# Performance work log

Hardware: AMD Instinct MI355X
Metric: run time of the kernel (lower is better)

Reference implementation:

```python
import jax, jax.numpy as jnp
import numpy as np

N_NODES = 100000


def _gcn_conv(h, src, dst, W, b, n_nodes):
    """PyG GCNConv with add_self_loops=True, symmetric normalization.
    out = D^-1/2 (A + I) D^-1/2 (h W) + b, aggregating src->dst."""
    h = h @ W  # transform first (out_dim <= in_dim), as PyG does
    ones = jnp.ones(src.shape[0], dtype=h.dtype)
    deg = jax.ops.segment_sum(ones, dst, num_segments=n_nodes) + 1.0  # +1 self loop
    dinv = jax.lax.rsqrt(deg)
    coef = dinv[src] * dinv[dst]  # per-edge norm
    agg = jax.ops.segment_sum(h[src] * coef[:, None], dst, num_segments=n_nodes)
    agg = agg + h * (dinv * dinv)[:, None]  # self-loop term: dinv_i^2 * h_i
    return agg + b


def setup_inputs() -> dict:
    key = jax.random.key(0)
    k1, k2, k3, k4 = jax.random.split(key, 4)
    x = jax.random.normal(k1, (N_NODES, 256), dtype=jnp.float32)
    edge_index = jax.random.randint(k2, (2, 1600000), 0, N_NODES, dtype=jnp.int64)
    W1 = jax.random.normal(k3, (256, 128), dtype=jnp.float32) * (1.0 / np.sqrt(256))
    b1 = jnp.zeros((128,), dtype=jnp.float32)
    W2 = jax.random.normal(k4, (128, 64), dtype=jnp.float32) * (1.0 / np.sqrt(128))
    b2 = jnp.zeros((64,), dtype=jnp.float32)
    return {"x": x, "edge_index": edge_index, "W1": W1, "b1": b1, "W2": W2, "b2": b2}


def reference(x, edge_index, W1, b1, W2, b2):
    src, dst = edge_index[0], edge_index[1]
    h = jax.nn.relu(_gcn_conv(x, src, dst, W1, b1, N_NODES))
    # dropout is identity in eval mode
    h = _gcn_conv(h, src, dst, W2, b2, N_NODES)
    return jax.nn.log_softmax(h, axis=1)
```

## Files before the change

### kernel.cpp

```cpp
#include <hip/hip_runtime.h>
#include <hip/hip_bf16.h>


#define N_NODES 100000
#define F_IN 256
#define F_MID 128
#define F_OUT 64

#define BSHIFT 8
#define BNODES 256
#define NBUCKETS ((N_NODES + BNODES - 1) / BNODES)
#define BCAP 6144
#define EPB 4096

typedef __attribute__((ext_vector_type(8))) short short8;
typedef __attribute__((ext_vector_type(4))) float f32x4;

__device__ inline ushort bf16_rne(float f) {
    uint u = __float_as_uint(f);
    u += 0x7FFF + ((u >> 16) & 1);
    return (ushort)(u >> 16);
}
__device__ inline float lo16(uint r) { return __uint_as_float(r << 16); }
__device__ inline float hi16(uint r) { return __uint_as_float(r & 0xffff0000u); }
__device__ inline uint pack_bf2(float a, float b) {
    return (uint)bf16_rne(a) | ((uint)bf16_rne(b) << 16);
}


__global__ __launch_bounds__(256)
void bucket_scatter_kernel(const int* __restrict__ src, const int* __restrict__ dst,
                           int* __restrict__ bcur, uint* __restrict__ ebuf, int E) {
    __shared__ int curL[NBUCKETS];
    int t = threadIdx.x;
    int e0 = blockIdx.x * EPB;
    int e1 = e0 + EPB; if (e1 > E) e1 = E;

    for (int i = t; i < NBUCKETS; i += 256) curL[i] = 0;
    __syncthreads();
    for (int i = e0 + t; i < e1; i += 256) atomicAdd(&curL[dst[i] >> BSHIFT], 1);
    __syncthreads();
    for (int i = t; i < NBUCKETS; i += 256) {
        int h = curL[i];
        curL[i] = h ? atomicAdd(&bcur[i], h) : 0;
    }
    __syncthreads();
    for (int i = e0 + t; i < e1; i += 256) {
        int d = dst[i], s = src[i];
        int b = d >> BSHIFT;
        int pos = atomicAdd(&curL[b], 1);
        if (pos < BCAP) ebuf[(size_t)b * BCAP + pos] = ((uint)(d & (BNODES - 1)) << 17) | (uint)s;
    }
}

__global__ __launch_bounds__(256)
void bucket_sort_kernel(const uint* __restrict__ ebuf, const int* __restrict__ bcur,
                        int* __restrict__ ssrc, int* __restrict__ rs, int* __restrict__ cnt,
                        float* __restrict__ dinv, int n) {
    __shared__ uint eL[BCAP];
    __shared__ int hist[BNODES], ps[BNODES];
    int b = blockIdx.x, t = threadIdx.x;
    int nb = bcur[b];
    if (nb > BCAP) nb = BCAP;
    for (int i = t; i < nb; i += 256) eL[i] = ebuf[(size_t)b * BCAP + i];
    hist[t] = 0;
    __syncthreads();
    for (int i = t; i < nb; i += 256) atomicAdd(&hist[eL[i] >> 17], 1);
    __syncthreads();
    ps[t] = hist[t];
    __syncthreads();
#pragma unroll
    for (int off = 1; off < BNODES; off <<= 1) {
        int v = (t >= off) ? ps[t - off] : 0;
        __syncthreads();
        ps[t] += v;
        __syncthreads();
    }
    int excl = ps[t] - hist[t];
    int node = b * BNODES + t;
    if (node < n) {
        rs[node] = b * BCAP + excl;
        cnt[node] = hist[t];
        dinv[node] = 1.0f / sqrtf((float)hist[t] + 1.0f);
    }
    __syncthreads();
    ps[t] = excl;
    __syncthreads();
    for (int i = t; i < nb; i += 256) {
        uint e = eL[i];
        int d = e >> 17;
        int p = atomicAdd(&ps[d], 1);
        ssrc[(size_t)b * BCAP + p] = (int)(e & 0x1FFFF);
    }
}

__global__ __launch_bounds__(256)
void wprep_kernel(const float* __restrict__ W1, const float* __restrict__ W2,
                  short8* __restrict__ W1f, short8* __restrict__ W2f) {
    int b = blockIdx.x;
    if (b < 16) {
        int f = b * 256 + threadIdx.x;
        int k0 = f >> 9, nt = (f >> 6) & 7, ln = f & 63;
        int kbase = k0 * 32 + (ln >> 4) * 8;
        int n = nt * 16 + (ln & 15);
        short8 fr;
#pragma unroll
        for (int j = 0; j < 8; ++j) fr[j] = (short)bf16_rne(W1[(kbase + j) * F_MID + n]);
        W1f[f] = fr;
    } else {
        int f = (b - 16) * 256 + threadIdx.x;
        int k0 = f >> 8, nt = (f >> 6) & 3, ln = f & 63;
        int kbase = k0 * 32 + (ln >> 4) * 8;
        int n = nt * 16 + (ln & 15);
        short8 fr;
#pragma unroll
        for (int j = 0; j < 8; ++j) fr[j] = (short)bf16_rne(W2[(kbase + j) * F_OUT + n]);
        W2f[f] = fr;
    }
}


__global__ __launch_bounds__(512, 2)
void gemm1_kernel(const float* __restrict__ A, const short8* __restrict__ Wf,
                  const float* __restrict__ dinv, ushort* __restrict__ C,
                  int M) {
    __shared__ short8 BsF[4096];
    __shared__ ushort Abuf[2][128 * 64];
    int tid = threadIdx.x;
    int lane = tid & 63, w = tid >> 6;
    int m0 = blockIdx.x * 128;

    int o0 = tid * 2;
    int srow = o0 >> 3;
    int gr = m0 + srow; if (gr >= M) gr = m0;
    int cl0 = o0 & 7, cl1 = cl0 + 1;
    int cg0 = cl0 ^ (srow & 7), cg1 = cl1 ^ (srow & 7);
    const float* arow = &A[(size_t)gr * F_IN];

    float4 rv[2][2];
    rv[0][0] = ((const float4*)(arow + cg0 * 8))[0];
    rv[0][1] = ((const float4*)(arow + cg0 * 8))[1];
    rv[1][0] = ((const float4*)(arow + cg1 * 8))[0];
    rv[1][1] = ((const float4*)(arow + cg1 * 8))[1];

    for (int f = tid; f < 4096; f += 512) BsF[f] = Wf[f];

    {
        short8 pk;
        pk[0] = (short)bf16_rne(rv[0][0].x); pk[1] = (short)bf16_rne(rv[0][0].y);
        pk[2] = (short)bf16_rne(rv[0][0].z); pk[3] = (short)bf16_rne(rv[0][0].w);
        pk[4] = (short)bf16_rne(rv[0][1].x); pk[5] = (short)bf16_rne(rv[0][1].y);
        pk[6] = (short)bf16_rne(rv[0][1].z); pk[7] = (short)bf16_rne(rv[0][1].w);
        *(short8*)&Abuf[0][o0 * 8] = pk;
        pk[0] = (short)bf16_rne(rv[1][0].x); pk[1] = (short)bf16_rne(rv[1][0].y);
        pk[2] = (short)bf16_rne(rv[1][0].z); pk[3] = (short)bf16_rne(rv[1][0].w);
        pk[4] = (short)bf16_rne(rv[1][1].x); pk[5] = (short)bf16_rne(rv[1][1].y);
        pk[6] = (short)bf16_rne(rv[1][1].z); pk[7] = (short)bf16_rne(rv[1][1].w);
        *(short8*)&Abuf[0][(o0 + 1) * 8] = pk;
    }
    __syncthreads();

    f32x4 acc[8];
#pragma unroll
    for (int nt = 0; nt < 8; ++nt) acc[nt] = (f32x4){0.f, 0.f, 0.f, 0.f};

    int arow16 = w * 16 + (lane & 15);
    int asw = arow16 & 7;
    int abase = arow16 * 8;

#pragma unroll
    for (int kc = 0; kc < 4; ++kc) {
        int b = kc & 1;
        if (kc < 3) {
            const float* s0 = arow + (kc + 1) * 64 + cg0 * 8;
            const float* s1 = arow + (kc + 1) * 64 + cg1 * 8;
            rv[0][0] = ((const float4*)s0)[0];
            rv[0][1] = ((const float4*)s0)[1];
            rv[1][0] = ((const float4*)s1)[0];
            rv[1][1] = ((const float4*)s1)[1];
            asm volatile("" ::: "memory");
        }
#pragma unroll
        for (int kk = 0; kk < 2; ++kk) {
            int k0 = kc * 2 + kk;
            int c = kk * 4 + (lane >> 4);
            short8 af = *(const short8*)&Abuf[b][(abase + (c ^ asw)) * 8];
#pragma unroll
            for (int nt = 0; nt < 8; ++nt) {
                short8 bfr = BsF[(k0 * 8 + nt) * 64 + lane];
                acc[nt] = __builtin_amdgcn_mfma_f32_16x16x32_bf16(af, bfr, acc[nt], 0, 0, 0);
            }
        }
        if (kc < 3) {
            short8 pk;
            pk[0] = (short)bf16_rne(rv[0][0].x); pk[1] = (short)bf16_rne(rv[0][0].y);
            pk[2] = (short)bf16_rne(rv[0][0].z); pk[3] = (short)bf16_rne(rv[0][0].w);
            pk[4] = (short)bf16_rne(rv[0][1].x); pk[5] = (short)bf16_rne(rv[0][1].y);
            pk[6] = (short)bf16_rne(rv[0][1].z); pk[7] = (short)bf16_rne(rv[0][1].w);
            *(short8*)&Abuf[b ^ 1][o0 * 8] = pk;
            pk[0] = (short)bf16_rne(rv[1][0].x); pk[1] = (short)bf16_rne(rv[1][0].y);
            pk[2] = (short)bf16_rne(rv[1][0].z); pk[3] = (short)bf16_rne(rv[1][0].w);
            pk[4] = (short)bf16_rne(rv[1][1].x); pk[5] = (short)bf16_rne(rv[1][1].y);
            pk[6] = (short)bf16_rne(rv[1][1].z); pk[7] = (short)bf16_rne(rv[1][1].w);
            *(short8*)&Abuf[b ^ 1][(o0 + 1) * 8] = pk;
        }
        __syncthreads();
    }

#pragma unroll
    for (int i = 0; i < 4; ++i) {
        int r = blockIdx.x * 128 + w * 16 + (lane >> 4) * 4 + i;
        if (r < M) {
            float dv = dinv[r];
#pragma unroll
            for (int nt = 0; nt < 8; ++nt)
                C[(size_t)r * F_MID + nt * 16 + (lane & 15)] = bf16_rne(dv * acc[nt][i]);
        }
    }
}

__global__ __launch_bounds__(512, 4)
void gemm2_kernel(const ushort* __restrict__ A, const short8* __restrict__ Wf,
                  const float* __restrict__ dinv, ushort* __restrict__ C,
                  int M) {
    __shared__ short8 BsF[1024];
    int tid = threadIdx.x;
    int lane = tid & 63, w = tid >> 6;
    for (int f = tid; f < 1024; f += 512) BsF[f] = Wf[f];
    __syncthreads();

    int m0 = blockIdx.x * 128 + w * 16;
    int m = m0 + (lane & 15);
    bool mOk = (m < M);

    f32x4 acc[4];
#pragma unroll
    for (int nt = 0; nt < 4; ++nt) acc[nt] = (f32x4){0.f, 0.f, 0.f, 0.f};

    short8 afr[4];
#pragma unroll
    for (int k0 = 0; k0 < 4; ++k0) {
        short8 af = (short8){0, 0, 0, 0, 0, 0, 0, 0};
        if (mOk) af = *(const short8*)&A[(size_t)m * F_MID + k0 * 32 + (lane >> 4) * 8];
        afr[k0] = af;
    }
#pragma unroll
    for (int k0 = 0; k0 < 4; ++k0)
#pragma unroll
        for (int nt = 0; nt < 4; ++nt) {
            short8 bfr = BsF[(k0 * 4 + nt) * 64 + lane];
            acc[nt] = __builtin_amdgcn_mfma_f32_16x16x32_bf16(afr[k0], bfr, acc[nt], 0, 0, 0);
        }
#pragma unroll
    for (int i = 0; i < 4; ++i) {
        int r = m0 + (lane >> 4) * 4 + i;
        if (r < M) {
            float dv = dinv[r];
#pragma unroll
            for (int nt = 0; nt < 4; ++nt)
                C[(size_t)r * F_OUT + nt * 16 + (lane & 15)] = bf16_rne(dv * acc[nt][i]);
        }
    }
}

__global__ __launch_bounds__(256)
void agg1_kernel(const uint4* __restrict__ h, const int* __restrict__ rs,
                 const int* __restrict__ cnt, const int* __restrict__ ssrc,
                 const float* __restrict__ dinv, const float* __restrict__ bias,
                 uint4* __restrict__ outp, int n) {
    int w = threadIdx.x >> 6, lane = threadIdx.x & 63;
    int node = blockIdx.x * 4 + w;
    if (node >= n) return;
    int q = lane >> 4, c16 = lane & 15;
    int start = rs[node], c = cnt[node];
    float dn = dinv[node];
    float a[8];
#pragma unroll
    for (int i = 0; i < 8; ++i) a[i] = 0.f;

    for (int base = 0; base < c; base += 16) {
        bool p[4];
        int s[4];
        uint4 r[4];
#pragma unroll
        for (int j = 0; j < 4; ++j) {
            int e = base + j * 4 + q;
            p[j] = e < c;
            if (p[j]) s[j] = ssrc[start + e];
        }
#pragma unroll
        for (int j = 0; j < 4; ++j)
            if (p[j]) r[j] = h[(size_t)s[j] * 16 + c16];
#pragma unroll
        for (int j = 0; j < 4; ++j) {
            if (p[j]) {
                a[0] += lo16(r[j].x); a[1] += hi16(r[j].x);
                a[2] += lo16(r[j].y); a[3] += hi16(r[j].y);
                a[4] += lo16(r[j].z); a[5] += hi16(r[j].z);
                a[6] += lo16(r[j].w); a[7] += hi16(r[j].w);
            }
        }
    }
#pragma unroll
    for (int i = 0; i < 8; ++i) {
        a[i] += __shfl_xor(a[i], 16);
        a[i] += __shfl_xor(a[i], 32);
    }
    uint4 sr = h[(size_t)node * 16 + c16];
    const float4* b4 = (const float4*)bias;
    float4 b0 = b4[c16 * 2], b1 = b4[c16 * 2 + 1];
    float o0 = fmaxf(fmaf(dn, a[0] + lo16(sr.x), b0.x), 0.f);
    float o1 = fmaxf(fmaf(dn, a[1] + hi16(sr.x), b0.y), 0.f);
    float o2 = fmaxf(fmaf(dn, a[2] + lo16(sr.y), b0.z), 0.f);
    float o3 = fmaxf(fmaf(dn, a[3] + hi16(sr.y), b0.w), 0.f);
    float o4 = fmaxf(fmaf(dn, a[4] + lo16(sr.z), b1.x), 0.f);
    float o5 = fmaxf(fmaf(dn, a[5] + hi16(sr.z), b1.y), 0.f);
    float o6 = fmaxf(fmaf(dn, a[6] + lo16(sr.w), b1.z), 0.f);
    float o7 = fmaxf(fmaf(dn, a[7] + hi16(sr.w), b1.w), 0.f);
    if (q == 0) {
        uint4 ov;
        ov.x = pack_bf2(o0, o1);
        ov.y = pack_bf2(o2, o3);
        ov.z = pack_bf2(o4, o5);
        ov.w = pack_bf2(o6, o7);
        outp[(size_t)node * 16 + c16] = ov;
    }
}

__global__ __launch_bounds__(256)
void agg2_kernel(const uint2* __restrict__ h, const int* __restrict__ rs,
                 const int* __restrict__ cnt, const int* __restrict__ ssrc,
                 const float* __restrict__ dinv, const float* __restrict__ bias,
                 float4* __restrict__ out4, int n) {
    int w = threadIdx.x >> 6, lane = threadIdx.x & 63;
    int node = blockIdx.x * 4 + w;
    if (node >= n) return;
    int q = lane >> 4, c16 = lane & 15;
    int start = rs[node], c = cnt[node];
    float dn = dinv[node];
    float a[4];
#pragma unroll
    for (int i = 0; i < 4; ++i) a[i] = 0.f;

    for (int base = 0; base < c; base += 16) {
        bool p[4];
        int s[4];
        uint2 r[4];
#pragma unroll
        for (int j = 0; j < 4; ++j) {
            int e = base + j * 4 + q;
            p[j] = e < c;
            if (p[j]) s[j] = ssrc[start + e];
        }
#pragma unroll
        for (int j = 0; j < 4; ++j)
            if (p[j]) r[j] = h[(size_t)s[j] * 16 + c16];
#pragma unroll
        for (int j = 0; j < 4; ++j) {
            if (p[j]) {
                a[0] += lo16(r[j].x); a[1] += hi16(r[j].x);
                a[2] += lo16(r[j].y); a[3] += hi16(r[j].y);
            }
        }
    }
#pragma unroll
    for (int i = 0; i < 4; ++i) {
        a[i] += __shfl_xor(a[i], 16);
        a[i] += __shfl_xor(a[i], 32);
    }
    uint2 sr = h[(size_t)node * 16 + c16];
    float4 bv = ((const float4*)bias)[c16];
    float v0 = fmaf(dn, a[0] + lo16(sr.x), bv.x);
    float v1 = fmaf(dn, a[1] + hi16(sr.x), bv.y);
    float v2 = fmaf(dn, a[2] + lo16(sr.y), bv.z);
    float v3 = fmaf(dn, a[3] + hi16(sr.y), bv.w);
    float m = fmaxf(fmaxf(v0, v1), fmaxf(v2, v3));
#pragma unroll
    for (int off = 1; off < 16; off <<= 1) m = fmaxf(m, __shfl_xor(m, off));
    float ssum = expf(v0 - m) + expf(v1 - m) + expf(v2 - m) + expf(v3 - m);
#pragma unroll
    for (int off = 1; off < 16; off <<= 1) ssum += __shfl_xor(ssum, off);
    float lg = m + logf(ssum);
    if (q == 0) out4[(size_t)node * 16 + c16] = make_float4(v0 - lg, v1 - lg, v2 - lg, v3 - lg);
}


extern "C" void kernel_launch(void* const* d_in, const int* in_sizes, int n_in,
                              void* d_out, int out_size, void* d_ws, size_t ws_size,
                              hipStream_t stream) {
    const float* x  = (const float*)d_in[0];
    const int*   ei = (const int*)d_in[1];
    const float* W1 = (const float*)d_in[2];
    const float* b1 = (const float*)d_in[3];
    const float* W2 = (const float*)d_in[4];
    const float* b2 = (const float*)d_in[5];
    float* out = (float*)d_out;

    const int N = N_NODES;
    const int E = in_sizes[1] / 2;
    const int* src = ei;
    const int* dst = ei + E;

    char* ws = (char*)d_ws;
    size_t off = 0;
    auto alloc = [&](size_t bytes) {
        char* p = ws + off;
        off = (off + bytes + 255) & ~(size_t)255;
        return p;
    };
    int*    bcur   = (int*)alloc(NBUCKETS * 4);
    int*    rs     = (int*)alloc(N * 4);
    int*    cnt    = (int*)alloc(N * 4);
    float*  dinv   = (float*)alloc(N * 4);
    short8* W1f    = (short8*)alloc(4096 * 16);
    short8* W2f    = (short8*)alloc(1024 * 16);
    uint*   ebuf   = (uint*)alloc((size_t)NBUCKETS * BCAP * 4);
    int*    ssrc   = (int*)alloc((size_t)NBUCKETS * BCAP * 4);
    uint*   h1     = (uint*)alloc((size_t)N * 64 * 4);
    uint*   h1a    = (uint*)alloc((size_t)N * 64 * 4);
    ushort* h2     = (ushort*)h1;

    const int nScatBlocks = (E + EPB - 1) / EPB;
    const int nAggBlocks  = (N + 3) / 4;
    const int nTiles      = (N + 127) / 128;

    hipMemsetAsync(bcur, 0, NBUCKETS * 4, stream);
    wprep_kernel<<<20, 256, 0, stream>>>(W1, W2, W1f, W2f);

    bucket_scatter_kernel<<<nScatBlocks, 256, 0, stream>>>(src, dst, bcur, ebuf, E);
    bucket_sort_kernel<<<NBUCKETS, 256, 0, stream>>>(ebuf, bcur, ssrc, rs, cnt, dinv, N);

    gemm1_kernel<<<nTiles, 512, 0, stream>>>(x, W1f, dinv, (ushort*)h1, N);
    agg1_kernel<<<nAggBlocks, 256, 0, stream>>>((const uint4*)h1, rs, cnt, ssrc, dinv, b1,
                                                (uint4*)h1a, N);
    gemm2_kernel<<<nTiles, 512, 0, stream>>>((const ushort*)h1a, W2f, dinv, h2, N);
    agg2_kernel<<<nAggBlocks, 256, 0, stream>>>((const uint2*)h2, rs, cnt, ssrc, dinv, b2,
                                                (float4*)out, N);
}
```

Baseline: 374.1 us.

## Fuse layer-1 aggregation with layer-2 GEMM via shared-memory row tile

```diff
diff --git a/kernel.cpp b/kernel.cpp
--- a/kernel.cpp
+++ b/kernel.cpp
@@ -219,111 +219,97 @@
     }
 }
 
-__global__ __launch_bounds__(512, 4)
-void gemm2_kernel(const ushort* __restrict__ A, const short8* __restrict__ Wf,
-                  const float* __restrict__ dinv, ushort* __restrict__ C,
-                  int M) {
-    __shared__ short8 BsF[1024];
-    int tid = threadIdx.x;
-    int lane = tid & 63, w = tid >> 6;
-    for (int f = tid; f < 1024; f += 512) BsF[f] = Wf[f];
-    __syncthreads();
-
-    int m0 = blockIdx.x * 128 + w * 16;
-    int m = m0 + (lane & 15);
-    bool mOk = (m < M);
-
-    f32x4 acc[4];
-#pragma unroll
-    for (int nt = 0; nt < 4; ++nt) acc[nt] = (f32x4){0.f, 0.f, 0.f, 0.f};
-
-    short8 afr[4];
+__global__ __launch_bounds__(256)
+void agg1f_kernel(const uint4* __restrict__ h, const int* __restrict__ rs,
+                  const int* __restrict__ cnt, const int* __restrict__ ssrc,
+                  const float* __restrict__ dinv, const float* __restrict__ bias,
+                  const short8* __restrict__ W2f, ushort* __restrict__ h2, int n) {
+    __shared__ __align__(16) ushort rowsL[16][136];
+    int w = threadIdx.x >> 6, lane = threadIdx.x & 63;
+    int q = lane >> 4, c16 = lane & 15;
+    int nbase = blockIdx.x * 16;
+    const float4* b4 = (const float4*)bias;
+    float4 b0 = b4[c16 * 2], b1v = b4[c16 * 2 + 1];
+
+#pragma unroll
+    for (int i = 0; i < 4; ++i) {
+        int node = nbase + w * 4 + i;
+        bool nOk = (node < n);
+        int start = nOk ? rs[node] : 0;
+        int c = nOk ? cnt[node] : 0;
+        float dn = nOk ? dinv[node] : 0.f;
+        float a[8];
+#pragma unroll
+        for (int k = 0; k < 8; ++k) a[k] = 0.f;
+
+        for (int base = 0; base < c; base += 16) {
+            bool p[4];
+            int s[4];
+            uint4 r[4];
+#pragma unroll
+            for (int j = 0; j < 4; ++j) {
+                int e = base + j * 4 + q;
+                p[j] = e < c;
+                if (p[j]) s[j] = ssrc[start + e];
+            }
+#pragma unroll
+            for (int j = 0; j < 4; ++j)
+                if (p[j]) r[j] = h[(size_t)s[j] * 16 + c16];
+#pragma unroll
+            for (int j = 0; j < 4; ++j) {
+                if (p[j]) {
+                    a[0] += lo16(r[j].x); a[1] += hi16(r[j].x);
+                    a[2] += lo16(r[j].y); a[3] += hi16(r[j].y);
+                    a[4] += lo16(r[j].z); a[5] += hi16(r[j].z);
+                    a[6] += lo16(r[j].w); a[7] += hi16(r[j].w);
+                }
+            }
+        }
+#pragma unroll
+        for (int k = 0; k < 8; ++k) {
+            a[k] += __shfl_xor(a[k], 16);
+            a[k] += __shfl_xor(a[k], 32);
+        }
+        if (q == 0) {
+            short8 pk;
+            if (nOk) {
+                uint4 sr = h[(size_t)node * 16 + c16];
+                float o0 = fmaxf(fmaf(dn, a[0] + lo16(sr.x), b0.x), 0.f);
+                float o1 = fmaxf(fmaf(dn, a[1] + hi16(sr.x), b0.y), 0.f);
+                float o2 = fmaxf(fmaf(dn, a[2] + lo16(sr.y), b0.z), 0.f);
+                float o3 = fmaxf(fmaf(dn, a[3] + hi16(sr.y), b0.w), 0.f);
+                float o4 = fmaxf(fmaf(dn, a[4] + lo16(sr.z), b1v.x), 0.f);
+                float o5 = fmaxf(fmaf(dn, a[5] + hi16(sr.z), b1v.y), 0.f);
+                float o6 = fmaxf(fmaf(dn, a[6] + lo16(sr.w), b1v.z), 0.f);
+                float o7 = fmaxf(fmaf(dn, a[7] + hi16(sr.w), b1v.w), 0.f);
+                pk[0] = (short)bf16_rne(o0); pk[1] = (short)bf16_rne(o1);
+                pk[2] = (short)bf16_rne(o2); pk[3] = (short)bf16_rne(o3);
+                pk[4] = (short)bf16_rne(o4); pk[5] = (short)bf16_rne(o5);
+                pk[6] = (short)bf16_rne(o6); pk[7] = (short)bf16_rne(o7);
+            } else {
+                pk = (short8){0, 0, 0, 0, 0, 0, 0, 0};
+            }
+            *(short8*)&rowsL[w * 4 + i][c16 * 8] = pk;
+        }
+    }
+    __syncthreads();
+
+    f32x4 acc = (f32x4){0.f, 0.f, 0.f, 0.f};
+    int ar = lane & 15;
 #pragma unroll
     for (int k0 = 0; k0 < 4; ++k0) {
-        short8 af = (short8){0, 0, 0, 0, 0, 0, 0, 0};
-        if (mOk) af = *(const short8*)&A[(size_t)m * F_MID + k0 * 32 + (lane >> 4) * 8];
-        afr[k0] = af;
-    }
-#pragma unroll
-    for (int k0 = 0; k0 < 4; ++k0)
-#pragma unroll
-        for (int nt = 0; nt < 4; ++nt) {
-            short8 bfr = BsF[(k0 * 4 + nt) * 64 + lane];
-            acc[nt] = __builtin_amdgcn_mfma_f32_16x16x32_bf16(afr[k0], bfr, acc[nt], 0, 0, 0);
-        }
+        short8 af = *(const short8*)&rowsL[ar][k0 * 32 + (lane >> 4) * 8];
+        short8 bfr = W2f[(k0 * 4 + w) * 64 + lane];
+        acc = __builtin_amdgcn_mfma_f32_16x16x32_bf16(af, bfr, acc, 0, 0, 0);
+    }
 #pragma unroll
     for (int i = 0; i < 4; ++i) {
-        int r = m0 + (lane >> 4) * 4 + i;
-        if (r < M) {
-            float dv = dinv[r];
-#pragma unroll
-            for (int nt = 0; nt < 4; ++nt)
-                C[(size_t)r * F_OUT + nt * 16 + (lane & 15)] = bf16_rne(dv * acc[nt][i]);
-        }
-    }
-}
-
-__global__ __launch_bounds__(256)
-void agg1_kernel(const uint4* __restrict__ h, const int* __restrict__ rs,
-                 const int* __restrict__ cnt, const int* __restrict__ ssrc,
-                 const float* __restrict__ dinv, const float* __restrict__ bias,
-                 uint4* __restrict__ outp, int n) {
-    int w = threadIdx.x >> 6, lane = threadIdx.x & 63;
-    int node = blockIdx.x * 4 + w;
-    if (node >= n) return;
-    int q = lane >> 4, c16 = lane & 15;
-    int start = rs[node], c = cnt[node];
-    float dn = dinv[node];
-    float a[8];
-#pragma unroll
-    for (int i = 0; i < 8; ++i) a[i] = 0.f;
-
-    for (int base = 0; base < c; base += 16) {
-        bool p[4];
-        int s[4];
-        uint4 r[4];
-#pragma unroll
-        for (int j = 0; j < 4; ++j) {
-            int e = base + j * 4 + q;
-            p[j] = e < c;
-            if (p[j]) s[j] = ssrc[start + e];
-        }
-#pragma unroll
-        for (int j = 0; j < 4; ++j)
-            if (p[j]) r[j] = h[(size_t)s[j] * 16 + c16];
-#pragma unroll
-        for (int j = 0; j < 4; ++j) {
-            if (p[j]) {
-                a[0] += lo16(r[j].x); a[1] += hi16(r[j].x);
-                a[2] += lo16(r[j].y); a[3] += hi16(r[j].y);
-                a[4] += lo16(r[j].z); a[5] += hi16(r[j].z);
-                a[6] += lo16(r[j].w); a[7] += hi16(r[j].w);
-            }
-        }
-    }
-#pragma unroll
-    for (int i = 0; i < 8; ++i) {
-        a[i] += __shfl_xor(a[i], 16);
-        a[i] += __shfl_xor(a[i], 32);
-    }
-    uint4 sr = h[(size_t)node * 16 + c16];
-    const float4* b4 = (const float4*)bias;
-    float4 b0 = b4[c16 * 2], b1 = b4[c16 * 2 + 1];
-    float o0 = fmaxf(fmaf(dn, a[0] + lo16(sr.x), b0.x), 0.f);
-    float o1 = fmaxf(fmaf(dn, a[1] + hi16(sr.x), b0.y), 0.f);
-    float o2 = fmaxf(fmaf(dn, a[2] + lo16(sr.y), b0.z), 0.f);
-    float o3 = fmaxf(fmaf(dn, a[3] + hi16(sr.y), b0.w), 0.f);
-    float o4 = fmaxf(fmaf(dn, a[4] + lo16(sr.z), b1.x), 0.f);
-    float o5 = fmaxf(fmaf(dn, a[5] + hi16(sr.z), b1.y), 0.f);
-    float o6 = fmaxf(fmaf(dn, a[6] + lo16(sr.w), b1.z), 0.f);
-    float o7 = fmaxf(fmaf(dn, a[7] + hi16(sr.w), b1.w), 0.f);
-    if (q == 0) {
-        uint4 ov;
-        ov.x = pack_bf2(o0, o1);
-        ov.y = pack_bf2(o2, o3);
-        ov.z = pack_bf2(o4, o5);
-        ov.w = pack_bf2(o6, o7);
-        outp[(size_t)node * 16 + c16] = ov;
+        int r = (lane >> 4) * 4 + i;
+        int node = nbase + r;
+        if (node < n) {
+            float dv = dinv[node];
+            h2[(size_t)node * F_OUT + w * 16 + (lane & 15)] = bf16_rne(dv * acc[i]);
+        }
     }
 }
 
@@ -417,11 +403,11 @@
     uint*   ebuf   = (uint*)alloc((size_t)NBUCKETS * BCAP * 4);
     int*    ssrc   = (int*)alloc((size_t)NBUCKETS * BCAP * 4);
     uint*   h1     = (uint*)alloc((size_t)N * 64 * 4);
-    uint*   h1a    = (uint*)alloc((size_t)N * 64 * 4);
-    ushort* h2     = (ushort*)h1;
+    ushort* h2     = (ushort*)alloc((size_t)N * 64 * 2);
 
     const int nScatBlocks = (E + EPB - 1) / EPB;
-    const int nAggBlocks  = (N + 3) / 4;
+    const int nAgg1Blocks = (N + 15) / 16;
+    const int nAgg2Blocks = (N + 3) / 4;
     const int nTiles      = (N + 127) / 128;
 
     hipMemsetAsync(bcur, 0, NBUCKETS * 4, stream);
@@ -431,9 +417,8 @@
     bucket_sort_kernel<<<NBUCKETS, 256, 0, stream>>>(ebuf, bcur, ssrc, rs, cnt, dinv, N);
 
     gemm1_kernel<<<nTiles, 512, 0, stream>>>(x, W1f, dinv, (ushort*)h1, N);
-    agg1_kernel<<<nAggBlocks, 256, 0, stream>>>((const uint4*)h1, rs, cnt, ssrc, dinv, b1,
-                                                (uint4*)h1a, N);
-    gemm2_kernel<<<nTiles, 512, 0, stream>>>((const ushort*)h1a, W2f, dinv, h2, N);
-    agg2_kernel<<<nAggBlocks, 256, 0, stream>>>((const uint2*)h2, rs, cnt, ssrc, dinv, b2,
-                                                (float4*)out, N);
-}
+    agg1f_kernel<<<nAgg1Blocks, 256, 0, stream>>>((const uint4*)h1, rs, cnt, ssrc, dinv, b1,
+                                                  W2f, h2, N);
+    agg2_kernel<<<nAgg2Blocks, 256, 0, stream>>>((const uint2*)h2, rs, cnt, ssrc, dinv, b2,
+                                                 (float4*)out, N);
+}
```

Result: no change. 367.8 us (-1.7%).
